# Kernel optimization log

Measured on AMD Instinct MI355X. Metric: run time of the kernel, lower is better.

Reference implementation:

```python
import jax, jax.numpy as jnp
import numpy as np

TEMPERATURE = 1.0
STRIDE = 1
PADDING = 2
RF = 5  # receptive_field_size
TREE_DEPTH = 3

# Each of the 16 binary difflogic ops op_g(a,b) is multilinear:
# op_g = c0 + c1*a + c2*b + c3*a*b. Rows ordered per the standard difflogic table:
# 0:0, 1:a&b, 2:a&~b, 3:a, 4:~a&b, 5:b, 6:xor, 7:or, 8:nor, 9:xnor,
# 10:~b, 11:a|~b, 12:~a, 13:~a|b, 14:nand, 15:1
_C = jnp.asarray(np.array([
    [0, 0, 0, 0],
    [0, 0, 0, 1],
    [0, 1, 0, -1],
    [0, 1, 0, 0],
    [0, 0, 1, -1],
    [0, 0, 1, 0],
    [0, 1, 1, -2],
    [0, 1, 1, -1],
    [1, -1, -1, 1],
    [1, -1, -1, 2],
    [1, 0, -1, 0],
    [1, 0, -1, 1],
    [1, -1, 0, 0],
    [1, -1, 0, 1],
    [1, 0, 0, -1],
    [1, 0, 0, 0]], dtype=np.float32))


def _gate(a, b, logits):
    """Soft LUT gate. a,b: (B,K,N,P); logits: (N,K,16) -> (B,K,N,P)."""
    w = jax.nn.softmax(logits / TEMPERATURE, axis=-1)          # (N,K,16)
    coef = jnp.einsum('nkg,gc->knc', w, _C)                    # (K,N,4)
    c = coef[None, :, :, None, :]                              # (1,K,N,1,4)
    return c[..., 0] + c[..., 1] * a + c[..., 2] * b + c[..., 3] * (a * b)


def setup_inputs() -> dict:
    key = jax.random.key(0)
    ks = jax.random.split(key, 8)
    B, Cin, H, W = 16, 32, 64, 64
    K, N = 64, 2 ** TREE_DEPTH  # num_kernels, leaf gates per tree
    x = jax.random.uniform(ks[0], (B, Cin, H, W), dtype=jnp.float32)
    idx_h = jax.random.randint(ks[1], (2, K, N), 0, RF, dtype=jnp.int32)
    idx_w = jax.random.randint(ks[2], (2, K, N), 0, RF, dtype=jnp.int32)
    idx_c = jax.random.randint(ks[3], (2, K, N), 0, Cin, dtype=jnp.int32)
    w0 = jax.random.normal(ks[4], (8, K, 16), dtype=jnp.float32)
    w1 = jax.random.normal(ks[5], (4, K, 16), dtype=jnp.float32)
    w2 = jax.random.normal(ks[6], (2, K, 16), dtype=jnp.float32)
    w3 = jax.random.normal(ks[7], (1, K, 16), dtype=jnp.float32)
    return {"x": x, "idx_h": idx_h, "idx_w": idx_w, "idx_c": idx_c,
            "w0": w0, "w1": w1, "w2": w2, "w3": w3}


def reference(x, idx_h, idx_w, idx_c, w0, w1, w2, w3):
    B, Cin, H, W = x.shape
    xp = jnp.pad(x, ((0, 0), (0, 0), (PADDING, PADDING), (PADDING, PADDING)))
    out_h = (H + 2 * PADDING - RF) // STRIDE + 1
    out_w = (W + 2 * PADDING - RF) // STRIDE + 1
    # Absolute gather coords per (rank-slot, kernel, leaf-gate, out_y, out_x)
    abs_h = idx_h[..., None, None] + (jnp.arange(out_h) * STRIDE)[:, None]   # (2,K,N,oh,1)
    abs_w = idx_w[..., None, None] + (jnp.arange(out_w) * STRIDE)[None, :]   # (2,K,N,1,ow)
    cc = idx_c[..., None, None]                                              # (2,K,N,1,1)
    g = xp[:, cc, abs_h, abs_w]                                # (B,2,K,N,oh,ow)
    K, N = g.shape[2], g.shape[3]
    g = g.reshape(B, 2, K, N, out_h * out_w)                   # (B,2,K,N,P)
    cur = _gate(g[:, 0], g[:, 1], w0)                          # (B,K,8,P) leaf level
    for wl in (w1, w2, w3):                                    # reduce tree: 8->4->2->1
        cur = _gate(cur[:, :, 0::2, :], cur[:, :, 1::2, :], wl)
    return cur.reshape(B, K, out_h, out_w)
```

## Files before the change

kernel.cpp:

```cpp
#include <hip/hip_runtime.h>
#include <hip/hip_bf16.h>

#define CIN 32
#define HW 64
#define KK 64
#define NLEAF 8
#define PADDING 2
#define TR 8
#define TC 16
#define WR 12
#define WC 20
#define WPOS (CIN * WR * WC)

typedef float f32x2 __attribute__((ext_vector_type(2)));

__device__ __constant__ float d_C[16][4] = {
    {0, 0, 0, 0},  {0, 0, 0, 1},  {0, 1, 0, -1}, {0, 1, 0, 0},
    {0, 0, 1, -1}, {0, 0, 1, 0},  {0, 1, 1, -2}, {0, 1, 1, -1},
    {1, -1, -1, 1},{1, -1, -1, 2},{1, 0, -1, 0}, {1, 0, -1, 1},
    {1, -1, 0, 0}, {1, -1, 0, 1}, {1, 0, 0, -1}, {1, 0, 0, 0}
};

__global__ __launch_bounds__(256) void prep_kernel(
    const int* __restrict__ idx_h, const int* __restrict__ idx_w, const int* __restrict__ idx_c,
    const float* __restrict__ w0, const float* __restrict__ w1,
    const float* __restrict__ w2, const float* __restrict__ w3,
    float* __restrict__ coefA, int* __restrict__ loffA)
{
    if (blockIdx.x == 4) {
        int k = threadIdx.x;
        if (k < KK) {
            #pragma unroll
            for (int n = 0; n < 16; ++n) {
                int s = n >> 3, leaf = n & 7;
                int o = s * (KK * NLEAF) + k * NLEAF + leaf;
                loffA[k * 16 + n] = idx_c[o] * (WR * WC) + idx_h[o] * WC + idx_w[o];
            }
        }
        return;
    }
    int t = blockIdx.x * blockDim.x + threadIdx.x;
    if (t >= KK * 15) return;
    int k = t / 15, node = t % 15;
    const float* wp; int n;
    if (node < 8)       { wp = w0; n = node; }
    else if (node < 12) { wp = w1; n = node - 8; }
    else if (node < 14) { wp = w2; n = node - 12; }
    else                { wp = w3; n = 0; }
    const float* l = wp + (n * KK + k) * 16;
    float m = l[0];
    #pragma unroll
    for (int g = 1; g < 16; ++g) m = fmaxf(m, l[g]);
    float p[16], s = 0.f;
    #pragma unroll
    for (int g = 0; g < 16; ++g) { p[g] = expf(l[g] - m); s += p[g]; }
    float inv = 1.f / s;
    float c0 = 0, c1 = 0, c2 = 0, c3 = 0;
    #pragma unroll
    for (int g = 0; g < 16; ++g) {
        float w = p[g] * inv;
        c0 = fmaf(w, d_C[g][0], c0);
        c1 = fmaf(w, d_C[g][1], c1);
        c2 = fmaf(w, d_C[g][2], c2);
        c3 = fmaf(w, d_C[g][3], c3);
    }
    float* o = coefA + (k * 60 + node * 4);
    o[0] = c0; o[1] = c1; o[2] = c2; o[3] = c3;
}

__device__ __forceinline__ f32x2 bc(float s) { return (f32x2){s, s}; }
__device__ __forceinline__ f32x2 gate2(const float* c, f32x2 a, f32x2 b) {
    return __builtin_elementwise_fma(b,
               __builtin_elementwise_fma(a, bc(c[3]), bc(c[2])),
               __builtin_elementwise_fma(a, bc(c[1]), bc(c[0])));
}

__global__ __launch_bounds__(512, 4) void logic_conv_kernel(
    const float* __restrict__ x, const int* __restrict__ loffA,
    const float* __restrict__ coefA, float* __restrict__ out)
{
    __shared__ f32x2 xt[WPOS];

    int tid = threadIdx.x;
    int bp  = blockIdx.x & 7;
    int rem = blockIdx.x >> 3;
    int t   = rem & 31;
    int kg  = rem >> 5;
    int r0  = (t >> 2) * TR;
    int c0  = (t & 3) * TC;

    const float* xb0 = x + (size_t)(2 * bp) * (CIN * HW * HW);
    const float* xb1 = xb0 + (CIN * HW * HW);

    #pragma unroll
    for (int i = 0; i < 15; ++i) {
        int e  = tid + i * 512;
        int c  = e / (WR * WC);
        int r  = e - c * (WR * WC);
        int rr = r / WC;
        int cc = r - rr * WC;
        int ih = r0 + rr - PADDING, iw = c0 + cc - PADDING;
        f32x2 v = {0.f, 0.f};
        if ((unsigned)ih < HW && (unsigned)iw < HW) {
            int go = (c * HW + ih) * HW + iw;
            v.x = xb0[go];
            v.y = xb1[go];
        }
        xt[e] = v;
    }
    __syncthreads();

    int lane = tid & 63, wave = tid >> 6;
    int tr = lane >> 4, tc = lane & 15;
    int pxe   = tr * WC + tc;
    int pxout = (r0 + tr) * HW + (c0 + tc);
    float* outB0 = out + ((size_t)(2 * bp) << 18);
    float* outB1 = outB0 + (1 << 18);

    int kbase = __builtin_amdgcn_readfirstlane(kg * 32 + wave * 4);

    #pragma unroll 2
    for (int i = 0; i < 4; ++i) {
        int k = kbase + i;
        const int*   L = loffA + (k << 4);
        const float* C = coefA + k * 60;

        f32x2 g0[16], g1[16];
        #pragma unroll
        for (int n = 0; n < 16; ++n) {
            const f32x2* p = &xt[L[n] + pxe];
            g0[n] = p[0];
            g1[n] = p[80];
        }

        f32x2 v0[8], v1[8];
        #pragma unroll
        for (int n = 0; n < 8; ++n) {
            v0[n] = gate2(C + 4 * n, g0[n], g0[8 + n]);
            v1[n] = gate2(C + 4 * n, g1[n], g1[8 + n]);
        }
        f32x2 u0[4], u1[4];
        #pragma unroll
        for (int n = 0; n < 4; ++n) {
            u0[n] = gate2(C + 32 + 4 * n, v0[2 * n], v0[2 * n + 1]);
            u1[n] = gate2(C + 32 + 4 * n, v1[2 * n], v1[2 * n + 1]);
        }
        f32x2 s00 = gate2(C + 48, u0[0], u0[1]);
        f32x2 s01 = gate2(C + 52, u0[2], u0[3]);
        f32x2 s10 = gate2(C + 48, u1[0], u1[1]);
        f32x2 s11 = gate2(C + 52, u1[2], u1[3]);
        f32x2 q0  = gate2(C + 56, s00, s01);
        f32x2 q1  = gate2(C + 56, s10, s11);

        int ko = (k << 12) + pxout;
        __builtin_nontemporal_store(q0.x, &outB0[ko]);
        __builtin_nontemporal_store(q0.y, &outB1[ko]);
        __builtin_nontemporal_store(q1.x, &outB0[ko + 4 * HW]);
        __builtin_nontemporal_store(q1.y, &outB1[ko + 4 * HW]);
    }
}

extern "C" void kernel_launch(void* const* d_in, const int* in_sizes, int n_in,
                              void* d_out, int out_size, void* d_ws, size_t ws_size,
                              hipStream_t stream) {
    const float* x     = (const float*)d_in[0];
    const int*   idx_h = (const int*)d_in[1];
    const int*   idx_w = (const int*)d_in[2];
    const int*   idx_c = (const int*)d_in[3];
    const float* w0    = (const float*)d_in[4];
    const float* w1    = (const float*)d_in[5];
    const float* w2    = (const float*)d_in[6];
    const float* w3    = (const float*)d_in[7];
    float* out   = (float*)d_out;

    float* coefA = (float*)d_ws;
    int*   loffA = (int*)((char*)d_ws + 16384);

    hipLaunchKernelGGL(prep_kernel, dim3(5), dim3(256), 0, stream,
                       idx_h, idx_w, idx_c, w0, w1, w2, w3, coefA, loffA);
    hipLaunchKernelGGL(logic_conv_kernel, dim3(512), dim3(512), 0, stream,
                       x, loffA, coefA, out);
}
```

Baseline: 24.16 us.

## Pack four batch images per LDS tile with shorter row tiles

The spatial tile shrinks from 8 to 4 output rows, and each block now stages four batch images, packed as float4 in shared memory, instead of two. Each thread computes one pixel row for four batches rather than two rows for two batches. This cuts the halo overhead per output for the batch dimension and allows one 16-byte LDS read per gather instead of two 8-byte reads. The cost is a larger vertical halo fraction (8 window rows for 4 output rows) and 20KB more dynamic shared memory, which may reduce occupancy.

```diff
diff --git a/kernel.cpp b/kernel.cpp
--- a/kernel.cpp
+++ b/kernel.cpp
@@ -6,13 +6,14 @@
 #define KK 64
 #define NLEAF 8
 #define PADDING 2
-#define TR 8
-#define TC 16
-#define WR 12
+#define TH 4
+#define TCW 16
+#define WR 8
 #define WC 20
 #define WPOS (CIN * WR * WC)
 
 typedef float f32x2 __attribute__((ext_vector_type(2)));
+typedef float f32x4 __attribute__((ext_vector_type(4)));
 
 __device__ __constant__ float d_C[16][4] = {
     {0, 0, 0, 0},  {0, 0, 0, 1},  {0, 1, 0, -1}, {0, 1, 0, 0},
@@ -79,32 +80,36 @@
     const float* __restrict__ x, const int* __restrict__ loffA,
     const float* __restrict__ coefA, float* __restrict__ out)
 {
-    __shared__ f32x2 xt[WPOS];
+    extern __shared__ f32x4 xt[];
 
-    int tid = threadIdx.x;
-    int bp  = blockIdx.x & 7;
-    int rem = blockIdx.x >> 3;
-    int t   = rem & 31;
-    int kg  = rem >> 5;
-    int r0  = (t >> 2) * TR;
-    int c0  = (t & 3) * TC;
+    int tid  = threadIdx.x;
+    int grp  = blockIdx.x & 7;
+    int quad = grp & 3;
+    int kh   = grp >> 2;
+    int t    = blockIdx.x >> 3;
+    int r0   = (t >> 2) * TH;
+    int c0   = (t & 3) * TCW;
 
-    const float* xb0 = x + (size_t)(2 * bp) * (CIN * HW * HW);
+    const float* xb0 = x + (size_t)(4 * quad) * (CIN * HW * HW);
     const float* xb1 = xb0 + (CIN * HW * HW);
+    const float* xb2 = xb1 + (CIN * HW * HW);
+    const float* xb3 = xb2 + (CIN * HW * HW);
 
     #pragma unroll
-    for (int i = 0; i < 15; ++i) {
+    for (int i = 0; i < 10; ++i) {
         int e  = tid + i * 512;
         int c  = e / (WR * WC);
         int r  = e - c * (WR * WC);
         int rr = r / WC;
         int cc = r - rr * WC;
         int ih = r0 + rr - PADDING, iw = c0 + cc - PADDING;
-        f32x2 v = {0.f, 0.f};
+        f32x4 v = {0.f, 0.f, 0.f, 0.f};
         if ((unsigned)ih < HW && (unsigned)iw < HW) {
             int go = (c * HW + ih) * HW + iw;
             v.x = xb0[go];
             v.y = xb1[go];
+            v.z = xb2[go];
+            v.w = xb3[go];
         }
         xt[e] = v;
     }
@@ -114,10 +119,12 @@
     int tr = lane >> 4, tc = lane & 15;
     int pxe   = tr * WC + tc;
     int pxout = (r0 + tr) * HW + (c0 + tc);
-    float* outB0 = out + ((size_t)(2 * bp) << 18);
+    float* outB0 = out + ((size_t)(4 * quad) << 18);
     float* outB1 = outB0 + (1 << 18);
+    float* outB2 = outB1 + (1 << 18);
+    float* outB3 = outB2 + (1 << 18);
 
-    int kbase = __builtin_amdgcn_readfirstlane(kg * 32 + wave * 4);
+    int kbase = __builtin_amdgcn_readfirstlane(kh * 32 + wave * 4);
 
     #pragma unroll 2
     for (int i = 0; i < 4; ++i) {
@@ -125,38 +132,38 @@
         const int*   L = loffA + (k << 4);
         const float* C = coefA + k * 60;
 
-        f32x2 g0[16], g1[16];
+        f32x2 gA[16], gB[16];
         #pragma unroll
         for (int n = 0; n < 16; ++n) {
-            const f32x2* p = &xt[L[n] + pxe];
-            g0[n] = p[0];
-            g1[n] = p[80];
+            f32x4 gv = xt[L[n] + pxe];
+            gA[n] = (f32x2){gv.x, gv.y};
+            gB[n] = (f32x2){gv.z, gv.w};
         }
 
-        f32x2 v0[8], v1[8];
+        f32x2 vA[8], vB[8];
         #pragma unroll
         for (int n = 0; n < 8; ++n) {
-            v0[n] = gate2(C + 4 * n, g0[n], g0[8 + n]);
-            v1[n] = gate2(C + 4 * n, g1[n], g1[8 + n]);
+            vA[n] = gate2(C + 4 * n, gA[n], gA[8 + n]);
+            vB[n] = gate2(C + 4 * n, gB[n], gB[8 + n]);
         }
-        f32x2 u0[4], u1[4];
+        f32x2 uA[4], uB[4];
         #pragma unroll
         for (int n = 0; n < 4; ++n) {
-            u0[n] = gate2(C + 32 + 4 * n, v0[2 * n], v0[2 * n + 1]);
-            u1[n] = gate2(C + 32 + 4 * n, v1[2 * n], v1[2 * n + 1]);
+            uA[n] = gate2(C + 32 + 4 * n, vA[2 * n], vA[2 * n + 1]);
+            uB[n] = gate2(C + 32 + 4 * n, vB[2 * n], vB[2 * n + 1]);
         }
-        f32x2 s00 = gate2(C + 48, u0[0], u0[1]);
-        f32x2 s01 = gate2(C + 52, u0[2], u0[3]);
-        f32x2 s10 = gate2(C + 48, u1[0], u1[1]);
-        f32x2 s11 = gate2(C + 52, u1[2], u1[3]);
-        f32x2 q0  = gate2(C + 56, s00, s01);
-        f32x2 q1  = gate2(C + 56, s10, s11);
+        f32x2 sA0 = gate2(C + 48, uA[0], uA[1]);
+        f32x2 sA1 = gate2(C + 52, uA[2], uA[3]);
+        f32x2 sB0 = gate2(C + 48, uB[0], uB[1]);
+        f32x2 sB1 = gate2(C + 52, uB[2], uB[3]);
+        f32x2 qA  = gate2(C + 56, sA0, sA1);
+        f32x2 qB  = gate2(C + 56, sB0, sB1);
 
         int ko = (k << 12) + pxout;
-        __builtin_nontemporal_store(q0.x, &outB0[ko]);
-        __builtin_nontemporal_store(q0.y, &outB1[ko]);
-        __builtin_nontemporal_store(q1.x, &outB0[ko + 4 * HW]);
-        __builtin_nontemporal_store(q1.y, &outB1[ko + 4 * HW]);
+        __builtin_nontemporal_store(qA.x, &outB0[ko]);
+        __builtin_nontemporal_store(qA.y, &outB1[ko]);
+        __builtin_nontemporal_store(qB.x, &outB2[ko]);
+        __builtin_nontemporal_store(qB.y, &outB3[ko]);
     }
 }
 
@@ -178,6 +185,7 @@
 
     hipLaunchKernelGGL(prep_kernel, dim3(5), dim3(256), 0, stream,
                        idx_h, idx_w, idx_c, w0, w1, w2, w3, coefA, loffA);
-    hipLaunchKernelGGL(logic_conv_kernel, dim3(512), dim3(512), 0, stream,
+    hipLaunchKernelGGL(logic_conv_kernel, dim3(512), dim3(512),
+                       WPOS * sizeof(f32x4), stream,
                        x, loffA, coefA, out);
 }
```

Result: faster. 21.30 us (-11.8%).
